# Kernel optimization log

Hardware: AMD Instinct MI355X
Metric: run time of the kernel (lower is better)

Reference implementation:

```python
import jax, jax.numpy as jnp
import numpy as np

B, S, D, DQKV = 4, 2048, 1024, 1024

def setup_inputs() -> dict:
    key = jax.random.key(0)
    kx, kq, kk, kv = jax.random.split(key, 4)
    scale = 1.0 / np.sqrt(D)
    return {
        "x": jax.random.normal(kx, (B, S, D), dtype=jnp.float32),
        "wq": jax.random.normal(kq, (D, DQKV), dtype=jnp.float32) * scale,
        "wk": jax.random.normal(kk, (D, DQKV), dtype=jnp.float32) * scale,
        "wv": jax.random.normal(kv, (D, DQKV), dtype=jnp.float32) * scale,
    }

def reference(x, wq, wk, wv):
    # QKV projections: [B,S,D] @ [D,Dqkv] -> [B,S,Dqkv]
    q = jnp.einsum('bsd,de->bse', x, wq)
    k = jnp.einsum('bsd,de->bse', x, wk)
    v = jnp.einsum('bsd,de->bse', x, wv)
    # scores: [B,S,S], scaled by sqrt(dim_qkv)
    scores = jnp.einsum('bik,bjk->bij', q, k) / jnp.sqrt(jnp.asarray(DQKV, dtype=x.dtype))
    attn = jax.nn.softmax(scores, axis=-1)
    # output: [B,S,Dqkv]
    return jnp.einsum('bij,bjd->bid', attn, v)
```

## Files before the change

### kernel.cpp

```cpp
#include <hip/hip_runtime.h>
#include <cstdint>
#include <cstddef>

typedef __bf16 bf16;
typedef __bf16 bf16x4 __attribute__((ext_vector_type(4)));
typedef __bf16 bf16x8 __attribute__((ext_vector_type(8)));
typedef float  f32x4  __attribute__((ext_vector_type(4)));

#define BATCH 4
#define SEQ   2048
#define DIM   1024
#define LDP   2112

__device__ __forceinline__ bf16 to_bf16(float f) {
    unsigned u = __builtin_bit_cast(unsigned, f);
    u += 0x7fffu + ((u >> 16) & 1u);
    unsigned short h = (unsigned short)(u >> 16);
    return __builtin_bit_cast(bf16, h);
}

__device__ __forceinline__ void load16_lds(const bf16* g, bf16* l) {
    __builtin_amdgcn_global_load_lds(
        (__attribute__((address_space(1))) void*)(g),
        (__attribute__((address_space(3))) void*)(l),
        16, 0, 0);
}

#define BARRIER() __builtin_amdgcn_s_barrier()
#define LGKM0()   asm volatile("s_waitcnt lgkmcnt(0)")
#define VM0()     asm volatile("s_waitcnt vmcnt(0)")
#define VM6()     asm volatile("s_waitcnt vmcnt(6)")


__device__ __forceinline__ void stage_half(
    const bf16* __restrict__ srcRow0, int ld, int k0, bf16* dstHalfBase)
{
    const int tid  = threadIdx.x;
    const int wave = tid >> 6;
    const int lane = tid & 63;
    const int rg   = lane >> 3;
    const int scoff = ((lane & 7) ^ rg) * 8;
#pragma unroll
    for (int j = 0; j < 2; ++j) {
        const int r = wave * 16 + j * 8;
        load16_lds(srcRow0 + (size_t)(r + rg) * ld + k0 + scoff,
                   dstHalfBase + r * 64);
    }
}

__device__ __forceinline__ void gemm_p3_core(
    const bf16* __restrict__ Ablk, const bf16* __restrict__ Bblk,
    int K, int lda, int ldb, bf16* As, bf16* Bs, f32x4 acc[4][4])
{
    const int tid  = threadIdx.x;
    const int lane = tid & 63;
    const int wave = tid >> 6;
    const int wr   = wave >> 1;
    const int wc   = wave & 1;
    const int r16  = lane & 15;
    const int g    = lane >> 4;
    const int r7   = r16 & 7;
    const int pk0  = ((g) ^ r7) * 8;
    const int pk1  = ((4 + g) ^ r7) * 8;
    const int arow = (wr * 64 + r16) * 64;
    const int brow = (wc * 64 + r16) * 64;
    const int NT   = K >> 6;

    stage_half(Ablk, lda, 0, As);
    stage_half(Ablk + (size_t)128 * lda, lda, 0, As + 8192);
    stage_half(Bblk, ldb, 0, Bs);
    stage_half(Ablk, lda, 64, As + 16384);
    stage_half(Ablk + (size_t)128 * lda, lda, 64, As + 16384 + 8192);
    stage_half(Bblk, ldb, 64, Bs + 8192);
    VM6();
    BARRIER();

    int c0 = 0, c2 = 2;
    for (int t = 0; t < NT; ++t) {
        bf16* Ac = As + c0 * 16384;
        bf16* Bc = Bs + c0 * 8192;

        bf16x8 a[4][2], b[4][2];
#pragma unroll
        for (int n = 0; n < 4; ++n) {
            b[n][0] = *(const bf16x8*)(Bc + brow + n * 1024 + pk0);
            b[n][1] = *(const bf16x8*)(Bc + brow + n * 1024 + pk1);
        }
#pragma unroll
        for (int m = 0; m < 4; ++m) {
            a[m][0] = *(const bf16x8*)(Ac + arow + m * 1024 + pk0);
            a[m][1] = *(const bf16x8*)(Ac + arow + m * 1024 + pk1);
        }
        if (t + 2 < NT) {
            const int k2 = (t + 2) << 6;
            bf16* An = As + c2 * 16384;
            bf16* Bn = Bs + c2 * 8192;
            stage_half(Ablk, lda, k2, An);
            stage_half(Ablk + (size_t)128 * lda, lda, k2, An + 8192);
            stage_half(Bblk, ldb, k2, Bn);
        }
        __builtin_amdgcn_s_setprio(1);
#pragma unroll
        for (int m = 0; m < 4; ++m)
#pragma unroll
            for (int n = 0; n < 4; ++n)
#pragma unroll
                for (int ks = 0; ks < 2; ++ks)
                    acc[m][n] = __builtin_amdgcn_mfma_f32_16x16x32_bf16(
                        a[m][ks], b[n][ks], acc[m][n], 0, 0, 0);
        __builtin_amdgcn_s_setprio(0);

        LGKM0();
        if (t + 1 < NT) {
            if (t + 2 < NT) { VM6(); } else { VM0(); }
        }
        BARRIER();
        c0 = (c0 == 2) ? 0 : c0 + 1;
        c2 = (c2 == 2) ? 0 : c2 + 1;
    }
}

__device__ __forceinline__ void write_c128n(
    bf16* __restrict__ Cb, int ldc, const f32x4 acc[4][4])
{
    const int lane = threadIdx.x & 63;
    const int wave = threadIdx.x >> 6;
    const int wr = wave >> 1, wc = wave & 1;
    const int r16 = lane & 15, g = lane >> 4;
    const int row0 = wr * 64 + g * 4;
    const int col0 = wc * 64 + r16;
#pragma unroll
    for (int m = 0; m < 4; ++m)
#pragma unroll
        for (int n = 0; n < 4; ++n)
#pragma unroll
            for (int rr = 0; rr < 4; ++rr)
                Cb[(size_t)(row0 + m * 16 + rr) * ldc + col0 + n * 16] =
                    to_bf16(acc[m][n][rr]);
}

__global__ __launch_bounds__(512, 2) void proj_qk_p3(
    const bf16* __restrict__ xb, const bf16* __restrict__ Wt,
    bf16* __restrict__ Q, bf16* __restrict__ Kb)
{
    __shared__ bf16 As[49152];
    __shared__ bf16 Bs[24576];
    f32x4 acc[4][4] = {};

    const int p = blockIdx.x;
    const int x = p & 7, s = p >> 3;
    const int my = x * 4 + (s >> 4);
    const int j  = s & 15;
    const bf16* Ab = xb + (size_t)my * 256 * DIM;
    const bf16* Bb = Wt + (size_t)((j >> 3) ? DIM * DIM : 0)
                        + (size_t)(j & 7) * 128 * DIM;
    bf16* dst = (j >> 3) ? Kb : Q;
    bf16* Cb = dst + (size_t)my * 256 * DIM + (size_t)(j & 7) * 128;

    gemm_p3_core(Ab, Bb, DIM, DIM, DIM, As, Bs, acc);
    write_c128n(Cb, DIM, acc);
}

__global__ __launch_bounds__(512, 2) void proj_v(
    const bf16* __restrict__ xb, const bf16* __restrict__ Wt,
    bf16* __restrict__ Vt)
{
    __shared__ bf16 As[49152];
    __shared__ bf16 Bs[24576];
    f32x4 acc[4][4] = {};

    const int p = blockIdx.x;
    const int x = p & 7, s = p >> 3;
    const int bz = x & 3;
    const int vx = (x >> 2) * 8 + (s & 7);
    const int vy = s >> 3;
    const bf16* Ab = Wt + (size_t)2 * DIM * DIM + (size_t)vy * 256 * DIM;
    const bf16* Bb = xb + (size_t)bz * SEQ * DIM + (size_t)vx * 128 * DIM;
    bf16* Cb = Vt + (size_t)bz * DIM * LDP + (size_t)vy * 256 * LDP
                  + (size_t)vx * 128;

    gemm_p3_core(Ab, Bb, DIM, DIM, DIM, As, Bs, acc);
    write_c128n(Cb, LDP, acc);
}

__global__ __launch_bounds__(512, 2) void gemm_scores_p3(
    const bf16* __restrict__ Qm, const bf16* __restrict__ Kb,
    bf16* __restrict__ P, float* __restrict__ lsum)
{
    __shared__ bf16 As[49152];
    __shared__ bf16 Bs[24576];
    f32x4 acc[4][4] = {};

    const int p = blockIdx.x;
    const int x = p & 7, s = p >> 3;
    const int bz = x & 3;
    const int by = (x >> 2) * 4 + (s >> 4);
    const int bx = s & 15;
    const bf16* Ab = Qm + (size_t)bz * SEQ * DIM + (size_t)by * 256 * DIM;
    const bf16* Bb = Kb + (size_t)bz * SEQ * DIM + (size_t)bx * 128 * DIM;
    gemm_p3_core(Ab, Bb, DIM, DIM, DIM, As, Bs, acc);

    bf16* Cb  = P + (size_t)bz * SEQ * LDP;
    float* ls = lsum + (size_t)bz * SEQ;
    const int lane = threadIdx.x & 63;
    const int wave = threadIdx.x >> 6;
    const int wr = wave >> 1, wc = wave & 1;
    const int r16 = lane & 15, g = lane >> 4;
    const int rowB = by * 256 + wr * 64 + g * 4;
    const int colB = bx * 128 + wc * 64 + r16;
#pragma unroll
    for (int m = 0; m < 4; ++m)
#pragma unroll
        for (int rr = 0; rr < 4; ++rr) {
            float sum = 0.0f;
#pragma unroll
            for (int n = 0; n < 4; ++n) {
                const float e = __expf(acc[m][n][rr] * 0.03125f);
                sum += e;
                Cb[(size_t)(rowB + m * 16 + rr) * LDP + colB + n * 16] = to_bf16(e);
            }
            sum += __shfl_xor(sum, 1);
            sum += __shfl_xor(sum, 2);
            sum += __shfl_xor(sum, 4);
            sum += __shfl_xor(sum, 8);
            if (r16 == 0)
                atomicAdd(ls + rowB + m * 16 + rr, sum);
        }
}

__global__ __launch_bounds__(512, 2) void gemm_pv_p3(
    const bf16* __restrict__ P, const bf16* __restrict__ Vt,
    float* __restrict__ C, const float* __restrict__ lsum)
{
    __shared__ bf16 As[49152];
    __shared__ bf16 Bs[24576];
    f32x4 acc[4][4] = {};

    const int p = blockIdx.x;
    const int x = p & 7, s = p >> 3;
    const int bz = x & 3;
    const int by = (x >> 2) * 4 + (s >> 3);
    const int bx = s & 7;
    const bf16* Ab = P  + (size_t)bz * SEQ * LDP + (size_t)by * 256 * LDP;
    const bf16* Bb = Vt + (size_t)bz * DIM * LDP + (size_t)bx * 128 * LDP;
    gemm_p3_core(Ab, Bb, SEQ, LDP, LDP, As, Bs, acc);

    float* Cb = C + (size_t)bz * SEQ * DIM;
    const float* ls = lsum + (size_t)bz * SEQ;
    const int lane = threadIdx.x & 63;
    const int wave = threadIdx.x >> 6;
    const int wr = wave >> 1, wc = wave & 1;
    const int r16 = lane & 15, g = lane >> 4;
    const int row0 = by * 256 + wr * 64 + g * 4;
    const int col0 = bx * 128 + wc * 64 + r16;
#pragma unroll
    for (int m = 0; m < 4; ++m)
#pragma unroll
        for (int rr = 0; rr < 4; ++rr) {
            const int row = row0 + m * 16 + rr;
            const float inv = __builtin_amdgcn_rcpf(ls[row]);
#pragma unroll
            for (int n = 0; n < 4; ++n)
                Cb[(size_t)row * DIM + col0 + n * 16] = acc[m][n][rr] * inv;
        }
}

__global__ __launch_bounds__(256) void prep(
    const float* __restrict__ x,  const float* __restrict__ wq,
    const float* __restrict__ wk, const float* __restrict__ wv,
    bf16* __restrict__ xb, bf16* __restrict__ Wt, float* __restrict__ lsum)
{
    __shared__ float tile[32][33];
    const int b = blockIdx.x;
    const int tid = threadIdx.x;
    if (b < 8192) {
        const size_t i = ((size_t)b * 256 + tid) * 4;
        const float4 v = *(const float4*)(x + i);
        bf16x4 o = { to_bf16(v.x), to_bf16(v.y), to_bf16(v.z), to_bf16(v.w) };
        *(bf16x4*)(xb + i) = o;
    } else if (b < 8192 + 3072) {
        const int t   = b - 8192;
        const int sel = t >> 10;
        const int n0  = (t & 31) * 32;
        const int k0  = ((t >> 5) & 31) * 32;
        const float* w = (sel == 0) ? wq : (sel == 1) ? wk : wv;
        const int tx = tid & 31, ty = tid >> 5;
#pragma unroll
        for (int j = 0; j < 32; j += 8)
            tile[ty + j][tx] = w[(size_t)(k0 + ty + j) * 1024 + n0 + tx];
        __syncthreads();
        bf16* dst = Wt + (size_t)sel * 1024 * 1024;
#pragma unroll
        for (int j = 0; j < 32; j += 8)
            dst[(size_t)(n0 + ty + j) * 1024 + k0 + tx] = to_bf16(tile[tx][ty + j]);
    } else {
#pragma unroll
        for (int i = 0; i < 32; ++i)
            lsum[i * 256 + tid] = 0.0f;
    }
}

extern "C" void kernel_launch(void* const* d_in, const int* in_sizes, int n_in,
                              void* d_out, int out_size, void* d_ws, size_t ws_size,
                              hipStream_t stream)
{
    const float* x  = (const float*)d_in[0];
    const float* wq = (const float*)d_in[1];
    const float* wk = (const float*)d_in[2];
    const float* wv = (const float*)d_in[3];
    float* out = (float*)d_out;
    char* ws = (char*)d_ws;

    bf16*  xb   = (bf16*)(ws);
    bf16*  Wt   = (bf16*)(ws + (16u << 20));
    bf16*  Q    = (bf16*)(ws + (22u << 20));
    bf16*  Kb   = (bf16*)(ws + (38u << 20));
    bf16*  Vt   = (bf16*)(ws + (54u << 20));
    bf16*  P    = (bf16*)(ws + (72u << 20));
    float* lsum = (float*)(ws + (108u << 20));

    prep<<<dim3(8192 + 3072 + 1), dim3(256), 0, stream>>>(
        x, wq, wk, wv, xb, Wt, lsum);

    proj_qk_p3<<<dim3(512), dim3(512), 0, stream>>>(xb, Wt, Q, Kb);
    proj_v<<<dim3(256), dim3(512), 0, stream>>>(xb, Wt, Vt);

    gemm_scores_p3<<<dim3(512), dim3(512), 0, stream>>>(Q, Kb, P, lsum);

    gemm_pv_p3<<<dim3(256), dim3(512), 0, stream>>>(P, Vt, out, lsum);
}
```

Baseline: 228.6 us.

## Enlarge GEMM tiles to 256x256 with K=32 stages and per-block row sums

Every GEMM now uses 256x256 output tiles: eight waves in a 2x4 arrangement, each owning 128x64, with a 32-wide K step in place of 64. This halves the number of blocks and raises arithmetic intensity per block. The atomicAdd row-sum accumulation is replaced by per-column-group partial sums written to a buffer and reduced in the PV kernel, which also removes the lsum zeroing in prep. In exchange, grids shrink to 128-256 blocks, which may underfill the 256 CUs. Each thread also holds twice as many accumulator registers, and the K=32 step doubles the number of barriers per unit of work.

```diff
diff --git a/kernel.cpp b/kernel.cpp
--- a/kernel.cpp
+++ b/kernel.cpp
@@ -29,90 +29,83 @@
 #define BARRIER() __builtin_amdgcn_s_barrier()
 #define LGKM0()   asm volatile("s_waitcnt lgkmcnt(0)")
 #define VM0()     asm volatile("s_waitcnt vmcnt(0)")
-#define VM6()     asm volatile("s_waitcnt vmcnt(6)")
-
-
-__device__ __forceinline__ void stage_half(
-    const bf16* __restrict__ srcRow0, int ld, int k0, bf16* dstHalfBase)
-{
-    const int tid  = threadIdx.x;
-    const int wave = tid >> 6;
-    const int lane = tid & 63;
-    const int rg   = lane >> 3;
-    const int scoff = ((lane & 7) ^ rg) * 8;
-#pragma unroll
-    for (int j = 0; j < 2; ++j) {
-        const int r = wave * 16 + j * 8;
-        load16_lds(srcRow0 + (size_t)(r + rg) * ld + k0 + scoff,
-                   dstHalfBase + r * 64);
-    }
-}
-
-__device__ __forceinline__ void gemm_p3_core(
+#define VM4()     asm volatile("s_waitcnt vmcnt(4)")
+
+
+__device__ __forceinline__ void stage_r32(
+    const bf16* __restrict__ srcRow0, int ld, int k0, bf16* dstBase)
+{
+    const int t = threadIdx.x;
+    const int r = t >> 2;
+    const int c = (t & 3) ^ ((r >> 1) & 3);
+    load16_lds(srcRow0 + (size_t)r * ld + k0 + c * 8,
+               dstBase + (t >> 6) * 512);
+}
+
+__device__ __forceinline__ void gemm_p3w_core(
     const bf16* __restrict__ Ablk, const bf16* __restrict__ Bblk,
-    int K, int lda, int ldb, bf16* As, bf16* Bs, f32x4 acc[4][4])
+    int K, int lda, int ldb, bf16* As, bf16* Bs, f32x4 acc[8][4])
 {
     const int tid  = threadIdx.x;
     const int lane = tid & 63;
     const int wave = tid >> 6;
-    const int wr   = wave >> 1;
-    const int wc   = wave & 1;
+    const int wr   = wave >> 2;
+    const int wc   = wave & 3;
     const int r16  = lane & 15;
     const int g    = lane >> 4;
-    const int r7   = r16 & 7;
-    const int pk0  = ((g) ^ r7) * 8;
-    const int pk1  = ((4 + g) ^ r7) * 8;
-    const int arow = (wr * 64 + r16) * 64;
-    const int brow = (wc * 64 + r16) * 64;
-    const int NT   = K >> 6;
-
-    stage_half(Ablk, lda, 0, As);
-    stage_half(Ablk + (size_t)128 * lda, lda, 0, As + 8192);
-    stage_half(Bblk, ldb, 0, Bs);
-    stage_half(Ablk, lda, 64, As + 16384);
-    stage_half(Ablk + (size_t)128 * lda, lda, 64, As + 16384 + 8192);
-    stage_half(Bblk, ldb, 64, Bs + 8192);
-    VM6();
+    const int NT   = K >> 5;
+
+    const int arow0 = wr * 128 + r16;
+    const int brow0 = wc * 64 + r16;
+
+    stage_r32(Ablk, lda, 0, As);
+    stage_r32(Ablk + (size_t)128 * lda, lda, 0, As + 4096);
+    stage_r32(Bblk, ldb, 0, Bs);
+    stage_r32(Bblk + (size_t)128 * ldb, ldb, 0, Bs + 4096);
+    stage_r32(Ablk, lda, 32, As + 8192);
+    stage_r32(Ablk + (size_t)128 * lda, lda, 32, As + 8192 + 4096);
+    stage_r32(Bblk, ldb, 32, Bs + 8192);
+    stage_r32(Bblk + (size_t)128 * ldb, ldb, 32, Bs + 8192 + 4096);
+    VM4();
     BARRIER();
 
     int c0 = 0, c2 = 2;
     for (int t = 0; t < NT; ++t) {
-        bf16* Ac = As + c0 * 16384;
+        bf16* Ac = As + c0 * 8192;
         bf16* Bc = Bs + c0 * 8192;
 
-        bf16x8 a[4][2], b[4][2];
+        bf16x8 a[8], b[4];
 #pragma unroll
         for (int n = 0; n < 4; ++n) {
-            b[n][0] = *(const bf16x8*)(Bc + brow + n * 1024 + pk0);
-            b[n][1] = *(const bf16x8*)(Bc + brow + n * 1024 + pk1);
-        }
-#pragma unroll
-        for (int m = 0; m < 4; ++m) {
-            a[m][0] = *(const bf16x8*)(Ac + arow + m * 1024 + pk0);
-            a[m][1] = *(const bf16x8*)(Ac + arow + m * 1024 + pk1);
+            const int R = brow0 + n * 16;
+            b[n] = *(const bf16x8*)(Bc + R * 32 + ((g ^ ((R >> 1) & 3)) * 8));
+        }
+#pragma unroll
+        for (int m = 0; m < 8; ++m) {
+            const int R = arow0 + m * 16;
+            a[m] = *(const bf16x8*)(Ac + R * 32 + ((g ^ ((R >> 1) & 3)) * 8));
         }
         if (t + 2 < NT) {
-            const int k2 = (t + 2) << 6;
-            bf16* An = As + c2 * 16384;
+            const int k2 = (t + 2) << 5;
+            bf16* An = As + c2 * 8192;
             bf16* Bn = Bs + c2 * 8192;
-            stage_half(Ablk, lda, k2, An);
-            stage_half(Ablk + (size_t)128 * lda, lda, k2, An + 8192);
-            stage_half(Bblk, ldb, k2, Bn);
+            stage_r32(Ablk, lda, k2, An);
+            stage_r32(Ablk + (size_t)128 * lda, lda, k2, An + 4096);
+            stage_r32(Bblk, ldb, k2, Bn);
+            stage_r32(Bblk + (size_t)128 * ldb, ldb, k2, Bn + 4096);
         }
         __builtin_amdgcn_s_setprio(1);
 #pragma unroll
-        for (int m = 0; m < 4; ++m)
+        for (int m = 0; m < 8; ++m)
 #pragma unroll
             for (int n = 0; n < 4; ++n)
-#pragma unroll
-                for (int ks = 0; ks < 2; ++ks)
-                    acc[m][n] = __builtin_amdgcn_mfma_f32_16x16x32_bf16(
-                        a[m][ks], b[n][ks], acc[m][n], 0, 0, 0);
+                acc[m][n] = __builtin_amdgcn_mfma_f32_16x16x32_bf16(
+                    a[m], b[n], acc[m][n], 0, 0, 0);
         __builtin_amdgcn_s_setprio(0);
 
         LGKM0();
         if (t + 1 < NT) {
-            if (t + 2 < NT) { VM6(); } else { VM0(); }
+            if (t + 2 < NT) { VM4(); } else { VM0(); }
         }
         BARRIER();
         c0 = (c0 == 2) ? 0 : c0 + 1;
@@ -120,17 +113,17 @@
     }
 }
 
-__device__ __forceinline__ void write_c128n(
-    bf16* __restrict__ Cb, int ldc, const f32x4 acc[4][4])
+__device__ __forceinline__ void write_c256w(
+    bf16* __restrict__ Cb, int ldc, const f32x4 acc[8][4])
 {
     const int lane = threadIdx.x & 63;
     const int wave = threadIdx.x >> 6;
-    const int wr = wave >> 1, wc = wave & 1;
+    const int wr = wave >> 2, wc = wave & 3;
     const int r16 = lane & 15, g = lane >> 4;
-    const int row0 = wr * 64 + g * 4;
+    const int row0 = wr * 128 + g * 4;
     const int col0 = wc * 64 + r16;
 #pragma unroll
-    for (int m = 0; m < 4; ++m)
+    for (int m = 0; m < 8; ++m)
 #pragma unroll
         for (int n = 0; n < 4; ++n)
 #pragma unroll
@@ -139,77 +132,77 @@
                     to_bf16(acc[m][n][rr]);
 }
 
-__global__ __launch_bounds__(512, 2) void proj_qk_p3(
+__global__ __launch_bounds__(512, 2) void proj_qk_w(
     const bf16* __restrict__ xb, const bf16* __restrict__ Wt,
     bf16* __restrict__ Q, bf16* __restrict__ Kb)
 {
-    __shared__ bf16 As[49152];
+    __shared__ bf16 As[24576];
     __shared__ bf16 Bs[24576];
-    f32x4 acc[4][4] = {};
+    f32x4 acc[8][4] = {};
 
     const int p = blockIdx.x;
     const int x = p & 7, s = p >> 3;
-    const int my = x * 4 + (s >> 4);
-    const int j  = s & 15;
+    const int my = x * 4 + (s >> 3);
+    const int j  = s & 7;
     const bf16* Ab = xb + (size_t)my * 256 * DIM;
-    const bf16* Bb = Wt + (size_t)((j >> 3) ? DIM * DIM : 0)
-                        + (size_t)(j & 7) * 128 * DIM;
-    bf16* dst = (j >> 3) ? Kb : Q;
-    bf16* Cb = dst + (size_t)my * 256 * DIM + (size_t)(j & 7) * 128;
-
-    gemm_p3_core(Ab, Bb, DIM, DIM, DIM, As, Bs, acc);
-    write_c128n(Cb, DIM, acc);
-}
-
-__global__ __launch_bounds__(512, 2) void proj_v(
+    const bf16* Bb = Wt + (size_t)((j >> 2) ? DIM * DIM : 0)
+                        + (size_t)(j & 3) * 256 * DIM;
+    bf16* dst = (j >> 2) ? Kb : Q;
+    bf16* Cb = dst + (size_t)my * 256 * DIM + (size_t)(j & 3) * 256;
+
+    gemm_p3w_core(Ab, Bb, DIM, DIM, DIM, As, Bs, acc);
+    write_c256w(Cb, DIM, acc);
+}
+
+__global__ __launch_bounds__(512, 2) void proj_v_w(
     const bf16* __restrict__ xb, const bf16* __restrict__ Wt,
     bf16* __restrict__ Vt)
 {
-    __shared__ bf16 As[49152];
+    __shared__ bf16 As[24576];
     __shared__ bf16 Bs[24576];
-    f32x4 acc[4][4] = {};
+    f32x4 acc[8][4] = {};
 
     const int p = blockIdx.x;
     const int x = p & 7, s = p >> 3;
     const int bz = x & 3;
-    const int vx = (x >> 2) * 8 + (s & 7);
-    const int vy = s >> 3;
+    const int vx = (x >> 2) * 4 + (s & 3);
+    const int vy = s >> 2;
     const bf16* Ab = Wt + (size_t)2 * DIM * DIM + (size_t)vy * 256 * DIM;
-    const bf16* Bb = xb + (size_t)bz * SEQ * DIM + (size_t)vx * 128 * DIM;
+    const bf16* Bb = xb + (size_t)bz * SEQ * DIM + (size_t)vx * 256 * DIM;
     bf16* Cb = Vt + (size_t)bz * DIM * LDP + (size_t)vy * 256 * LDP
-                  + (size_t)vx * 128;
-
-    gemm_p3_core(Ab, Bb, DIM, DIM, DIM, As, Bs, acc);
-    write_c128n(Cb, LDP, acc);
-}
-
-__global__ __launch_bounds__(512, 2) void gemm_scores_p3(
+                  + (size_t)vx * 256;
+
+    gemm_p3w_core(Ab, Bb, DIM, DIM, DIM, As, Bs, acc);
+    write_c256w(Cb, LDP, acc);
+}
+
+__global__ __launch_bounds__(512, 2) void gemm_scores_w(
     const bf16* __restrict__ Qm, const bf16* __restrict__ Kb,
-    bf16* __restrict__ P, float* __restrict__ lsum)
-{
-    __shared__ bf16 As[49152];
+    bf16* __restrict__ P, float* __restrict__ lsumP)
+{
+    __shared__ bf16 As[24576];
     __shared__ bf16 Bs[24576];
-    f32x4 acc[4][4] = {};
+    __shared__ float rbuf[256][4];
+    f32x4 acc[8][4] = {};
 
     const int p = blockIdx.x;
     const int x = p & 7, s = p >> 3;
     const int bz = x & 3;
-    const int by = (x >> 2) * 4 + (s >> 4);
-    const int bx = s & 15;
+    const int by = (x >> 2) * 4 + (s >> 3);
+    const int bxg = s & 7;
     const bf16* Ab = Qm + (size_t)bz * SEQ * DIM + (size_t)by * 256 * DIM;
-    const bf16* Bb = Kb + (size_t)bz * SEQ * DIM + (size_t)bx * 128 * DIM;
-    gemm_p3_core(Ab, Bb, DIM, DIM, DIM, As, Bs, acc);
-
-    bf16* Cb  = P + (size_t)bz * SEQ * LDP;
-    float* ls = lsum + (size_t)bz * SEQ;
+    const bf16* Bb = Kb + (size_t)bz * SEQ * DIM + (size_t)bxg * 256 * DIM;
+    gemm_p3w_core(Ab, Bb, DIM, DIM, DIM, As, Bs, acc);
+
+    bf16* Cb = P + (size_t)bz * SEQ * LDP;
     const int lane = threadIdx.x & 63;
     const int wave = threadIdx.x >> 6;
-    const int wr = wave >> 1, wc = wave & 1;
+    const int wr = wave >> 2, wc = wave & 3;
     const int r16 = lane & 15, g = lane >> 4;
-    const int rowB = by * 256 + wr * 64 + g * 4;
-    const int colB = bx * 128 + wc * 64 + r16;
-#pragma unroll
-    for (int m = 0; m < 4; ++m)
+    const int rowL0 = wr * 128 + g * 4;
+    const int colB  = bxg * 256 + wc * 64 + r16;
+#pragma unroll
+    for (int m = 0; m < 8; ++m)
 #pragma unroll
         for (int rr = 0; rr < 4; ++rr) {
             float sum = 0.0f;
@@ -217,48 +210,67 @@
             for (int n = 0; n < 4; ++n) {
                 const float e = __expf(acc[m][n][rr] * 0.03125f);
                 sum += e;
-                Cb[(size_t)(rowB + m * 16 + rr) * LDP + colB + n * 16] = to_bf16(e);
+                Cb[(size_t)(by * 256 + rowL0 + m * 16 + rr) * LDP
+                   + colB + n * 16] = to_bf16(e);
             }
             sum += __shfl_xor(sum, 1);
             sum += __shfl_xor(sum, 2);
             sum += __shfl_xor(sum, 4);
             sum += __shfl_xor(sum, 8);
             if (r16 == 0)
-                atomicAdd(ls + rowB + m * 16 + rr, sum);
-        }
-}
-
-__global__ __launch_bounds__(512, 2) void gemm_pv_p3(
+                rbuf[rowL0 + m * 16 + rr][wc] = sum;
+        }
+    BARRIER();
+    if (threadIdx.x < 256) {
+        const int r = threadIdx.x;
+        const float tot = rbuf[r][0] + rbuf[r][1] + rbuf[r][2] + rbuf[r][3];
+        lsumP[((size_t)bz * 8 + bxg) * SEQ + by * 256 + r] = tot;
+    }
+}
+
+__global__ __launch_bounds__(512, 2) void gemm_pv_w(
     const bf16* __restrict__ P, const bf16* __restrict__ Vt,
-    float* __restrict__ C, const float* __restrict__ lsum)
-{
-    __shared__ bf16 As[49152];
+    float* __restrict__ C, const float* __restrict__ lsumP)
+{
+    __shared__ bf16 As[24576];
     __shared__ bf16 Bs[24576];
-    f32x4 acc[4][4] = {};
+    __shared__ float sbuf[256];
+    f32x4 acc[8][4] = {};
 
     const int p = blockIdx.x;
     const int x = p & 7, s = p >> 3;
     const int bz = x & 3;
-    const int by = (x >> 2) * 4 + (s >> 3);
-    const int bx = s & 7;
+    const int by = (x >> 2) * 4 + (s >> 2);
+    const int bxg = s & 3;
     const bf16* Ab = P  + (size_t)bz * SEQ * LDP + (size_t)by * 256 * LDP;
-    const bf16* Bb = Vt + (size_t)bz * DIM * LDP + (size_t)bx * 128 * LDP;
-    gemm_p3_core(Ab, Bb, SEQ, LDP, LDP, As, Bs, acc);
+    const bf16* Bb = Vt + (size_t)bz * DIM * LDP + (size_t)bxg * 256 * LDP;
+    gemm_p3w_core(Ab, Bb, SEQ, LDP, LDP, As, Bs, acc);
+
+    if (threadIdx.x < 256) {
+        const int r = threadIdx.x;
+        const size_t base = (size_t)bz * 8 * SEQ + by * 256 + r;
+        float t = 0.0f;
+#pragma unroll
+        for (int jj = 0; jj < 8; ++jj)
+            t += lsumP[base + (size_t)jj * SEQ];
+        sbuf[r] = t;
+    }
+    BARRIER();
 
     float* Cb = C + (size_t)bz * SEQ * DIM;
-    const float* ls = lsum + (size_t)bz * SEQ;
     const int lane = threadIdx.x & 63;
     const int wave = threadIdx.x >> 6;
-    const int wr = wave >> 1, wc = wave & 1;
+    const int wr = wave >> 2, wc = wave & 3;
     const int r16 = lane & 15, g = lane >> 4;
-    const int row0 = by * 256 + wr * 64 + g * 4;
-    const int col0 = bx * 128 + wc * 64 + r16;
-#pragma unroll
-    for (int m = 0; m < 4; ++m)
+    const int rowL0 = wr * 128 + g * 4;
+    const int col0  = bxg * 256 + wc * 64 + r16;
+#pragma unroll
+    for (int m = 0; m < 8; ++m)
 #pragma unroll
         for (int rr = 0; rr < 4; ++rr) {
-            const int row = row0 + m * 16 + rr;
-            const float inv = __builtin_amdgcn_rcpf(ls[row]);
+            const int rl = rowL0 + m * 16 + rr;
+            const float inv = __builtin_amdgcn_rcpf(sbuf[rl]);
+            const int row = by * 256 + rl;
 #pragma unroll
             for (int n = 0; n < 4; ++n)
                 Cb[(size_t)row * DIM + col0 + n * 16] = acc[m][n][rr] * inv;
@@ -268,7 +280,7 @@
 __global__ __launch_bounds__(256) void prep(
     const float* __restrict__ x,  const float* __restrict__ wq,
     const float* __restrict__ wk, const float* __restrict__ wv,
-    bf16* __restrict__ xb, bf16* __restrict__ Wt, float* __restrict__ lsum)
+    bf16* __restrict__ xb, bf16* __restrict__ Wt)
 {
     __shared__ float tile[32][33];
     const int b = blockIdx.x;
@@ -278,7 +290,7 @@
         const float4 v = *(const float4*)(x + i);
         bf16x4 o = { to_bf16(v.x), to_bf16(v.y), to_bf16(v.z), to_bf16(v.w) };
         *(bf16x4*)(xb + i) = o;
-    } else if (b < 8192 + 3072) {
+    } else {
         const int t   = b - 8192;
         const int sel = t >> 10;
         const int n0  = (t & 31) * 32;
@@ -293,10 +305,6 @@
 #pragma unroll
         for (int j = 0; j < 32; j += 8)
             dst[(size_t)(n0 + ty + j) * 1024 + k0 + tx] = to_bf16(tile[tx][ty + j]);
-    } else {
-#pragma unroll
-        for (int i = 0; i < 32; ++i)
-            lsum[i * 256 + tid] = 0.0f;
     }
 }
 
@@ -311,21 +319,21 @@
     float* out = (float*)d_out;
     char* ws = (char*)d_ws;
 
-    bf16*  xb   = (bf16*)(ws);
-    bf16*  Wt   = (bf16*)(ws + (16u << 20));
-    bf16*  Q    = (bf16*)(ws + (22u << 20));
-    bf16*  Kb   = (bf16*)(ws + (38u << 20));
-    bf16*  Vt   = (bf16*)(ws + (54u << 20));
-    bf16*  P    = (bf16*)(ws + (72u << 20));
-    float* lsum = (float*)(ws + (108u << 20));
-
-    prep<<<dim3(8192 + 3072 + 1), dim3(256), 0, stream>>>(
-        x, wq, wk, wv, xb, Wt, lsum);
-
-    proj_qk_p3<<<dim3(512), dim3(512), 0, stream>>>(xb, Wt, Q, Kb);
-    proj_v<<<dim3(256), dim3(512), 0, stream>>>(xb, Wt, Vt);
-
-    gemm_scores_p3<<<dim3(512), dim3(512), 0, stream>>>(Q, Kb, P, lsum);
-
-    gemm_pv_p3<<<dim3(256), dim3(512), 0, stream>>>(P, Vt, out, lsum);
-}
+    bf16*  xb    = (bf16*)(ws);
+    bf16*  Wt    = (bf16*)(ws + (16u << 20));
+    bf16*  Q     = (bf16*)(ws + (22u << 20));
+    bf16*  Kb    = (bf16*)(ws + (38u << 20));
+    bf16*  Vt    = (bf16*)(ws + (54u << 20));
+    bf16*  P     = (bf16*)(ws + (72u << 20));
+    float* lsumP = (float*)(ws + (108u << 20));
+
+    prep<<<dim3(8192 + 3072), dim3(256), 0, stream>>>(
+        x, wq, wk, wv, xb, Wt);
+
+    proj_qk_w<<<dim3(256), dim3(512), 0, stream>>>(xb, Wt, Q, Kb);
+    proj_v_w<<<dim3(128), dim3(512), 0, stream>>>(xb, Wt, Vt);
+
+    gemm_scores_w<<<dim3(256), dim3(512), 0, stream>>>(Q, Kb, P, lsumP);
+
+    gemm_pv_w<<<dim3(128), dim3(512), 0, stream>>>(P, Vt, out, lsumP);
+}
```

Result: slower. 242.4 us (+6.0%).
